# Kernel optimization log

Hardware: AMD Instinct MI355X
Metric: run time of the kernel (lower is better)

## Reference

```python
import jax, jax.numpy as jnp
import numpy as np

N_USER, N_VIDEO, N_PUB, N_TAG = 200000, 100000, 20000, 5000
EMB = 128
HALF = EMB // 2
LAYER_NUM = 3


def setup_inputs() -> dict:
    key = jax.random.key(0)
    ks = jax.random.split(key, 20)
    inp = {
        "user_emb": jax.random.normal(ks[0], (N_USER, EMB), jnp.float32),
        "video_emb": jax.random.normal(ks[1], (N_VIDEO, EMB), jnp.float32),
        "publisher_emb": jax.random.normal(ks[2], (N_PUB, EMB), jnp.float32),
        "tag_emb": jax.random.normal(ks[3], (N_TAG, EMB), jnp.float32),
    }
    # (name, E, n_src, n_dst)
    rels = [
        ("uv", 1500000, N_USER, N_VIDEO),
        ("vu", 1500000, N_VIDEO, N_USER),
        ("up", 800000, N_USER, N_PUB),
        ("pu", 800000, N_PUB, N_USER),
        ("vt", 800000, N_VIDEO, N_TAG),
        ("tv", 800000, N_TAG, N_VIDEO),
        ("pt", 400000, N_PUB, N_TAG),
        ("tp", 400000, N_TAG, N_PUB),
    ]
    for i, (name, E, ns, nd) in enumerate(rels):
        inp[name + "_src"] = jax.random.randint(ks[4 + 2 * i], (E,), 0, ns, jnp.int32)
        inp[name + "_dst"] = jax.random.randint(ks[5 + 2 * i], (E,), 0, nd, jnp.int32)
    return inp


def _seg_mean(feat, src, dst, num_dst):
    # copy_u + mean: gather half-dim src features, segment-mean onto dst.
    msg = feat[src]                                             # [E, HALF]
    s = jax.ops.segment_sum(msg, dst, num_segments=num_dst)     # [num_dst, HALF]
    deg = jax.ops.segment_sum(jnp.ones_like(dst, dtype=feat.dtype), dst,
                              num_segments=num_dst)
    return s / jnp.maximum(deg, 1.0)[:, None]  # zero-in-degree nodes -> 0 (DGL behavior)


def reference(user_emb, video_emb, publisher_emb, tag_emb,
              uv_src, uv_dst, vu_src, vu_dst,
              up_src, up_dst, pu_src, pu_dst,
              vt_src, vt_dst, tv_src, tv_dst,
              pt_src, pt_dst, tp_src, tp_dst):

    def layer(u, v, p, t):
        # user dst: [vu, pu]; video dst: [uv, tv]; publisher dst: [up, tp]; tag dst: [vt, pt]
        vu = _seg_mean(v[:, :HALF], vu_src, vu_dst, N_USER)
        pu = _seg_mean(p[:, :HALF], pu_src, pu_dst, N_USER)
        uv = _seg_mean(u[:, :HALF], uv_src, uv_dst, N_VIDEO)
        tv = _seg_mean(t[:, :HALF], tv_src, tv_dst, N_VIDEO)
        up = _seg_mean(u[:, HALF:], up_src, up_dst, N_PUB)
        tp = _seg_mean(t[:, HALF:], tp_src, tp_dst, N_PUB)
        vt = _seg_mean(v[:, HALF:], vt_src, vt_dst, N_TAG)
        pt = _seg_mean(p[:, HALF:], pt_src, pt_dst, N_TAG)
        return (jnp.concatenate([vu, pu], axis=1),
                jnp.concatenate([uv, tv], axis=1),
                jnp.concatenate([up, tp], axis=1),
                jnp.concatenate([vt, pt], axis=1))

    pu_, pv_, pp_, pt_ = user_emb, video_emb, publisher_emb, tag_emb
    u, v, p, t = user_emb, video_emb, publisher_emb, tag_emb
    for i in range(LAYER_NUM):
        u, v, p, t = layer(u, v, p, t)
        w = 1.0 / (i + 2)
        pu_ = pu_ + u * w
        pv_ = pv_ + v * w
        pp_ = pp_ + p * w
        pt_ = pt_ + t * w
    return (pu_, pv_, pp_, pt_)
```

## Files before the change

kernel.cpp:

```cpp
#include <hip/hip_runtime.h>
#include <stdint.h>

#define EMB 128
#define PCAP 12288
#define SCAP 13312

static constexpr int N_USER = 200000, N_VIDEO = 100000, N_PUB = 20000, N_TAG = 5000;
static constexpr int ROW_U = 0, ROW_V = 200000, ROW_P = 300000, ROW_T = 320000;
static constexpr int ROWS = 325000;
static constexpr int TOTAL_E = 7000000;
static constexpr int TOTAL_GROUPS = 650000;
static constexpr int TILE = 8192;
static constexpr int SORT_MAX = TOTAL_E + 7 * TOTAL_GROUPS;

using f32x4 = __attribute__((ext_vector_type(4))) float;
using u32x4 = __attribute__((ext_vector_type(4))) unsigned int;
using u32x2 = __attribute__((ext_vector_type(2))) unsigned int;

__device__ inline unsigned bf16_rne(float f) {
  unsigned u = __float_as_uint(f);
  return (u + 0x7fffu + ((u >> 16) & 1u)) >> 16;
}
__device__ inline unsigned pack_bf16x2(float lo, float hi) {
  return bf16_rne(lo) | (bf16_rne(hi) << 16);
}

__device__ inline unsigned fp8enc(float f) {
  unsigned b = __float_as_uint(f);
  unsigned s = (b >> 24) & 0x80u;
  unsigned ae = b & 0x7FFFFFFFu;
  unsigned r = ae + 0x7FFFFu + ((ae >> 20) & 1u);
  unsigned e = r >> 23;
  if (e < 121u) {
    float av = __uint_as_float(ae);
    unsigned m = (unsigned)__builtin_rintf(av * 512.0f);
    return s | m;
  }
  return s | ((e - 120u) << 3) | ((r >> 20) & 7u);
}
#if __has_builtin(__builtin_amdgcn_cvt_f32_fp8)
#define DEC4(w, x0, x1, x2, x3) \
  x0 += __builtin_amdgcn_cvt_f32_fp8((int)(w), 0); \
  x1 += __builtin_amdgcn_cvt_f32_fp8((int)(w), 1); \
  x2 += __builtin_amdgcn_cvt_f32_fp8((int)(w), 2); \
  x3 += __builtin_amdgcn_cvt_f32_fp8((int)(w), 3);
#else
__device__ inline float fp8dec(unsigned b) {
  unsigned s = (b & 0x80u) << 24;
  unsigned e = (b >> 3) & 0xFu;
  unsigned m = b & 7u;
  if (e == 0) { float f = (float)m * 0.001953125f; return s ? -f : f; }
  return __uint_as_float(s | ((e + 120u) << 23) | (m << 20));
}
#define DEC4(w, x0, x1, x2, x3) \
  x0 += fp8dec((w) & 0xffu); x1 += fp8dec(((w) >> 8) & 0xffu); \
  x2 += fp8dec(((w) >> 16) & 0xffu); x3 += fp8dec(((w) >> 24) & 0xffu);
#endif

struct SortDesc {
  int tcum[9];
  int bcum[9];
  int gcum[8];
  int E[8];
  int n_dst[8];
  int wshift[8];
  int zrow[8];
  const int* esrc[8];
  const int* edst[8];
};

struct AggrDesc {
  int cum[9];
  int src_base[8];
  int src_col[8];
  int dst_base[8];
  int dst_col[8];
  const float* demb[8];
};

__global__ __launch_bounds__(256) void part_kernel(SortDesc d, unsigned* __restrict__ pairs,
                                                   int* __restrict__ cursors) {
  __shared__ int cnt[256];
  __shared__ int lcur[256];
  int blk = blockIdx.x;
  int r = 0;
#pragma unroll
  for (int k = 1; k < 8; ++k) if (blk >= d.tcum[k]) r = k;
  int base = (blk - d.tcum[r]) * TILE;
  int n = min(TILE, d.E[r] - base);
  const int* __restrict__ esrc = d.esrc[r];
  const int* __restrict__ edst = d.edst[r];
  int tid = threadIdx.x;
  int B = d.bcum[r + 1] - d.bcum[r];
  int sh = d.wshift[r];
  int msk = (1 << sh) - 1;
  int bb = d.bcum[r];
  if (tid < B) cnt[tid] = 0;
  __syncthreads();
  for (int i = tid; i < n; i += 256)
    atomicAdd(&cnt[edst[base + i] >> sh], 1);
  __syncthreads();
  if (tid < B) {
    int c = cnt[tid];
    lcur[tid] = c ? atomicAdd(&cursors[bb + tid], c) : 0;
  }
  __syncthreads();
  for (int i = tid; i < n; i += 256) {
    int dv = edst[base + i];
    int sv = esrc[base + i];
    int b = dv >> sh;
    int pos = atomicAdd(&lcur[b], 1);
    if (pos < PCAP)
      pairs[(size_t)(bb + b) * PCAP + pos] = ((unsigned)(dv & msk) << 18) | (unsigned)sv;
  }
}

__global__ __launch_bounds__(256) void build_kernel(SortDesc d, const unsigned* __restrict__ pairs,
                                                    const int* __restrict__ cursors,
                                                    int* __restrict__ gcounter,
                                                    int* __restrict__ sorted,
                                                    int* __restrict__ Beg, int* __restrict__ Deg) {
  __shared__ int cnt[1024];
  __shared__ int poff[1025];
  __shared__ int stage[SCAP];
  __shared__ int wsums[4];
  __shared__ int sh_gbase;
  int bucket = blockIdx.x;
  int r = 0;
#pragma unroll
  for (int k = 1; k < 8; ++k) if (bucket >= d.bcum[k]) r = k;
  int bl = bucket - d.bcum[r];
  int sh = d.wshift[r];
  int first = bl << sh;
  int Wa = min(1 << sh, d.n_dst[r] - first);
  int zr = d.zrow[r];
  int tid = threadIdx.x;
  int n_b = min(cursors[bucket], PCAP);
  const unsigned* __restrict__ bp = pairs + (size_t)bucket * PCAP;

  for (int i = tid; i < 1024; i += 256) cnt[i] = 0;
  __syncthreads();
  for (int i = tid; i < n_b; i += 256)
    atomicAdd(&cnt[bp[i] >> 18], 1);
  __syncthreads();

  int t4 = tid * 4;
  int c0 = cnt[t4], c1 = cnt[t4 + 1], c2 = cnt[t4 + 2], c3 = cnt[t4 + 3];
  int p0 = (c0 + 7) & ~7, p1 = (c1 + 7) & ~7, p2 = (c2 + 7) & ~7, p3 = (c3 + 7) & ~7;
  int s = p0 + p1 + p2 + p3;
  int lane = tid & 63, wv = tid >> 6;
  int v = s;
#pragma unroll
  for (int dd = 1; dd < 64; dd <<= 1) {
    int t = __shfl_up(v, dd);
    if (lane >= dd) v += t;
  }
  if (lane == 63) wsums[wv] = v;
  __syncthreads();
  if (tid == 0) {
    int run = 0;
#pragma unroll
    for (int k = 0; k < 4; ++k) { int t = wsums[k]; wsums[k] = run; run += t; }
  }
  __syncthreads();
  int ex = wsums[wv] + (v - s);
  if (tid == 255) {
    int tot = ex + s;
    sh_gbase = atomicAdd(gcounter, tot);
    poff[1024] = min(tot, SCAP);
  }
  __syncthreads();
  int gbase = sh_gbase;
  int o0 = ex, o1 = ex + p0, o2 = o1 + p1, o3 = o2 + p2;
  cnt[t4] = o0; cnt[t4 + 1] = o1; cnt[t4 + 2] = o2; cnt[t4 + 3] = o3;
  poff[t4] = o0; poff[t4 + 1] = o1; poff[t4 + 2] = o2; poff[t4 + 3] = o3;
  int g0 = d.gcum[r] + first + t4;
  if (t4 + 0 < Wa) { Beg[g0 + 0] = gbase + o0; Deg[g0 + 0] = c0; }
  if (t4 + 1 < Wa) { Beg[g0 + 1] = gbase + o1; Deg[g0 + 1] = c1; }
  if (t4 + 2 < Wa) { Beg[g0 + 2] = gbase + o2; Deg[g0 + 2] = c2; }
  if (t4 + 3 < Wa) { Beg[g0 + 3] = gbase + o3; Deg[g0 + 3] = c3; }
  __syncthreads();

  for (int i = tid; i < n_b; i += 256) {
    unsigned pr = bp[i];
    int pos = atomicAdd(&cnt[pr >> 18], 1);
    if (pos < SCAP) stage[pos] = (int)(pr & 0x3FFFFu);
  }
  __syncthreads();
#pragma unroll
  for (int jj = 0; jj < 4; ++jj) {
    int j = t4 + jj;
    int end_ = min((j < 1023) ? poff[j + 1] : poff[1024], SCAP);
    for (int k = cnt[j]; k < end_; ++k) stage[k] = zr;
  }
  __syncthreads();

  int tot = poff[1024];
  for (int i = tid; i < tot; i += 256)
    sorted[gbase + i] = stage[i];
}

__global__ void convert_kernel(const float* __restrict__ u, const float* __restrict__ v,
                               const float* __restrict__ p, const float* __restrict__ t,
                               uint16_t* __restrict__ featA, uint16_t* __restrict__ featB,
                               unsigned char* __restrict__ f1f8) {
  int idx = blockIdx.x * blockDim.x + threadIdx.x;
  const int total8 = (ROWS + 1) * EMB / 8;
  if (idx >= total8) return;
  int flat = idx * 8;
  int row = flat >> 7;
  if (row == ROWS) {
    uint4 z = {0u, 0u, 0u, 0u};
    *(uint4*)(featA + flat) = z;
    *(uint4*)(featB + flat) = z;
    if (f1f8) { uint2 z2 = {0u, 0u}; *(uint2*)(f1f8 + flat) = z2; }
    return;
  }
  int col = flat & 127;
  const float* s;
  if (row < ROW_V)      s = u + (size_t)row * EMB + col;
  else if (row < ROW_P) s = v + (size_t)(row - ROW_V) * EMB + col;
  else if (row < ROW_T) s = p + (size_t)(row - ROW_P) * EMB + col;
  else                  s = t + (size_t)(row - ROW_T) * EMB + col;
  float4 f0 = *(const float4*)s;
  float4 f1 = *((const float4*)s + 1);
  uint4 o;
  o.x = pack_bf16x2(f0.x, f0.y);
  o.y = pack_bf16x2(f0.z, f0.w);
  o.z = pack_bf16x2(f1.x, f1.y);
  o.w = pack_bf16x2(f1.z, f1.w);
  *(uint4*)(featA + flat) = o;
}

#define ACC(q) \
  a0 += __uint_as_float((q).x << 16); a1 += __uint_as_float((q).x & 0xffff0000u); \
  a2 += __uint_as_float((q).y << 16); a3 += __uint_as_float((q).y & 0xffff0000u); \
  a4 += __uint_as_float((q).z << 16); a5 += __uint_as_float((q).z & 0xffff0000u); \
  a6 += __uint_as_float((q).w << 16); a7 += __uint_as_float((q).w & 0xffff0000u);

#define ACC8(qq) \
  DEC4((qq).x, a0, a1, a2, a3); DEC4((qq).y, a4, a5, a6, a7);

template<int M>
__global__ __launch_bounds__(256) void aggr_kernel(AggrDesc d,
    const uint16_t* __restrict__ gsrc_bf, const unsigned char* __restrict__ gsrc_f8,
    uint16_t* __restrict__ dst_bf, unsigned char* __restrict__ dst_f8,
    const uint16_t* __restrict__ f1_bf, const uint16_t* __restrict__ demb_bf,
    float* __restrict__ out,
    const int* __restrict__ sorted, const int* __restrict__ Beg,
    const int* __restrict__ Deg) {
  if ((M == 1 || M == 3) && blockIdx.x == 0 && threadIdx.x < 16) {
    uint2 z = {0u, 0u};
    *(uint2*)(dst_f8 + (size_t)ROWS * EMB + threadIdx.x * 8) = z;
  }
  int g = blockIdx.x * 32 + (threadIdx.x >> 3);
  if (g >= TOTAL_GROUPS) return;
  int lane = threadIdx.x & 7;
  int r = 0;
#pragma unroll
  for (int k = 1; k < 8; ++k) if (g >= d.cum[k]) r = k;
  int n = g - d.cum[r];
  int beg = Beg[g], dg = Deg[g];
  float recip = 1.0f / (float)(dg > 0 ? dg : 1);
  constexpr bool GB = (M == 0 || M == 3 || M == 4);
  const uint16_t* __restrict__ sb16 =
      GB ? gsrc_bf + (size_t)d.src_base[r] * EMB + d.src_col[r] + lane * 8 : nullptr;
  const unsigned char* __restrict__ sb8 =
      !GB ? gsrc_f8 + (size_t)d.src_base[r] * EMB + d.src_col[r] + lane * 8 : nullptr;
  float a0 = 0.f, a1 = 0.f, a2 = 0.f, a3 = 0.f, a4 = 0.f, a5 = 0.f, a6 = 0.f, a7 = 0.f;
  int nchunk = (dg + 7) >> 3;
  const int* ep = sorted + beg;
  int4 iA0 = {0,0,0,0}, iA1 = {0,0,0,0};
  if (nchunk > 0) { iA0 = *(const int4*)ep; iA1 = *(const int4*)(ep + 4); }
  for (int c = 0; c < nchunk; ++c) {
    int4 iB0 = {0,0,0,0}, iB1 = {0,0,0,0};
    if (c + 1 < nchunk) { iB0 = *(const int4*)(ep + 8); iB1 = *(const int4*)(ep + 12); }
    if (GB) {
      uint4 q0 = *(const uint4*)(sb16 + (size_t)iA0.x * EMB);
      uint4 q1 = *(const uint4*)(sb16 + (size_t)iA0.y * EMB);
      uint4 q2 = *(const uint4*)(sb16 + (size_t)iA0.z * EMB);
      uint4 q3 = *(const uint4*)(sb16 + (size_t)iA0.w * EMB);
      uint4 q4 = *(const uint4*)(sb16 + (size_t)iA1.x * EMB);
      uint4 q5 = *(const uint4*)(sb16 + (size_t)iA1.y * EMB);
      uint4 q6 = *(const uint4*)(sb16 + (size_t)iA1.z * EMB);
      uint4 q7 = *(const uint4*)(sb16 + (size_t)iA1.w * EMB);
      __builtin_amdgcn_sched_barrier(0);
      ACC(q0); ACC(q1); ACC(q2); ACC(q3);
      ACC(q4); ACC(q5); ACC(q6); ACC(q7);
    } else {
      uint2 q0 = *(const uint2*)(sb8 + (size_t)iA0.x * EMB);
      uint2 q1 = *(const uint2*)(sb8 + (size_t)iA0.y * EMB);
      uint2 q2 = *(const uint2*)(sb8 + (size_t)iA0.z * EMB);
      uint2 q3 = *(const uint2*)(sb8 + (size_t)iA0.w * EMB);
      uint2 q4 = *(const uint2*)(sb8 + (size_t)iA1.x * EMB);
      uint2 q5 = *(const uint2*)(sb8 + (size_t)iA1.y * EMB);
      uint2 q6 = *(const uint2*)(sb8 + (size_t)iA1.z * EMB);
      uint2 q7 = *(const uint2*)(sb8 + (size_t)iA1.w * EMB);
      __builtin_amdgcn_sched_barrier(0);
      ACC8(q0); ACC8(q1); ACC8(q2); ACC8(q3);
      ACC8(q4); ACC8(q5); ACC8(q6); ACC8(q7);
    }
    iA0 = iB0; iA1 = iB1; ep += 8;
  }
  a0 *= recip; a1 *= recip; a2 *= recip; a3 *= recip;
  a4 *= recip; a5 *= recip; a6 *= recip; a7 *= recip;

  int col = d.dst_col[r] + lane * 8;
  size_t dpos = (size_t)(d.dst_base[r] + n) * EMB + col;

  if (M == 0 || M == 4) {
    u32x4 ov;
    ov.x = pack_bf16x2(a0, a1);
    ov.y = pack_bf16x2(a2, a3);
    ov.z = pack_bf16x2(a4, a5);
    ov.w = pack_bf16x2(a6, a7);
    __builtin_nontemporal_store(ov, (u32x4*)(dst_bf + dpos));
    if (M == 4) {
      u32x2 o8;
      o8.x = fp8enc(a0) | (fp8enc(a1) << 8) | (fp8enc(a2) << 16) | (fp8enc(a3) << 24);
      o8.y = fp8enc(a4) | (fp8enc(a5) << 8) | (fp8enc(a6) << 16) | (fp8enc(a7) << 24);
      __builtin_nontemporal_store(o8, (u32x2*)(dst_f8 + dpos));
    }
    return;
  }
  if (M == 1 || M == 3) {
    u32x2 ov;
    ov.x = fp8enc(a0) | (fp8enc(a1) << 8) | (fp8enc(a2) << 16) | (fp8enc(a3) << 24);
    ov.y = fp8enc(a4) | (fp8enc(a5) << 8) | (fp8enc(a6) << 16) | (fp8enc(a7) << 24);
    __builtin_nontemporal_store(ov, (u32x2*)(dst_f8 + dpos));
    return;
  }

  u32x4 q1 = __builtin_nontemporal_load((const u32x4*)(f1_bf + dpos));
  u32x2 qf = __builtin_nontemporal_load((const u32x2*)(gsrc_f8 + dpos));
  float g0 = 0.f, g1 = 0.f, g2 = 0.f, g3 = 0.f, g4 = 0.f, g5 = 0.f, g6 = 0.f, g7 = 0.f;
  DEC4(qf.x, g0, g1, g2, g3);
  DEC4(qf.y, g4, g5, g6, g7);
  f32x4 v0, v1;
  if (demb_bf) {
    u32x4 qe = __builtin_nontemporal_load((const u32x4*)(demb_bf + dpos));
    v0.x = __uint_as_float(qe.x << 16); v0.y = __uint_as_float(qe.x & 0xffff0000u);
    v0.z = __uint_as_float(qe.y << 16); v0.w = __uint_as_float(qe.y & 0xffff0000u);
    v1.x = __uint_as_float(qe.z << 16); v1.y = __uint_as_float(qe.z & 0xffff0000u);
    v1.z = __uint_as_float(qe.w << 16); v1.w = __uint_as_float(qe.w & 0xffff0000u);
  } else {
    const f32x4* de = (const f32x4*)(d.demb[r] + (size_t)n * EMB + col);
    v0 = __builtin_nontemporal_load(de);
    v1 = __builtin_nontemporal_load(de + 1);
  }
  const float w1 = 0.5f, w2 = 1.0f / 3.0f, w3 = 0.25f;
  v0.x += w1 * __uint_as_float(q1.x << 16)         + w2 * g0 + w3 * a0;
  v0.y += w1 * __uint_as_float(q1.x & 0xffff0000u) + w2 * g1 + w3 * a1;
  v0.z += w1 * __uint_as_float(q1.y << 16)         + w2 * g2 + w3 * a2;
  v0.w += w1 * __uint_as_float(q1.y & 0xffff0000u) + w2 * g3 + w3 * a3;
  v1.x += w1 * __uint_as_float(q1.z << 16)         + w2 * g4 + w3 * a4;
  v1.y += w1 * __uint_as_float(q1.z & 0xffff0000u) + w2 * g5 + w3 * a5;
  v1.z += w1 * __uint_as_float(q1.w << 16)         + w2 * g6 + w3 * a6;
  v1.w += w1 * __uint_as_float(q1.w & 0xffff0000u) + w2 * g7 + w3 * a7;
  __builtin_nontemporal_store(v0, (f32x4*)(out + dpos));
  __builtin_nontemporal_store(v1, (f32x4*)(out + dpos) + 1);
}

extern "C" void kernel_launch(void* const* d_in, const int* in_sizes, int n_in,
                              void* d_out, int out_size, void* d_ws, size_t ws_size,
                              hipStream_t stream) {
  const float* emb_u = (const float*)d_in[0];
  const float* emb_v = (const float*)d_in[1];
  const float* emb_p = (const float*)d_in[2];
  const float* emb_t = (const float*)d_in[3];

  struct RelInfo { int si, di, E, n_dst, src_base, src_col, dst_base, dst_col, wshift; };
  const RelInfo rels[8] = {
    {12, 13,  800000, N_TAG,   ROW_V, 64, ROW_T,  0,  5},
    {16, 17,  400000, N_TAG,   ROW_P, 64, ROW_T, 64,  5},
    { 8,  9,  800000, N_PUB,   ROW_U, 64, ROW_P,  0,  7},
    {18, 19,  400000, N_PUB,   ROW_T, 64, ROW_P, 64,  7},
    { 4,  5, 1500000, N_VIDEO, ROW_U,  0, ROW_V,  0,  9},
    {14, 15,  800000, N_VIDEO, ROW_T,  0, ROW_V, 64,  9},
    { 6,  7, 1500000, N_USER,  ROW_V,  0, ROW_U,  0, 10},
    {10, 11,  800000, N_USER,  ROW_P,  0, ROW_U, 64, 10},
  };
  const float* dembs[8] = {emb_t, emb_t, emb_p, emb_p, emb_v, emb_v, emb_u, emb_u};

  char* ws = (char*)d_ws;
  size_t cursor = 0;
  auto take = [&](size_t bytes) -> char* {
    char* p = ws + cursor;
    cursor = (cursor + bytes + 255) & ~(size_t)255;
    return p;
  };
  uint16_t* featA = (uint16_t*)take((size_t)(ROWS + 1) * EMB * 2);
  uint16_t* featB = (uint16_t*)take((size_t)(ROWS + 1) * EMB * 2);
  int* sorted = (int*)take((size_t)SORT_MAX * 4);
  int* Beg    = (int*)take((size_t)TOTAL_GROUPS * 4);
  int* Deg    = (int*)take((size_t)TOTAL_GROUPS * 4);
  unsigned* pairs = (unsigned*)d_ws;

  SortDesc sd;
  AggrDesc ad;
  int tacc = 0, bacc = 0, gacc = 0;
  for (int r = 0; r < 8; ++r) {
    int n_dst = rels[r].n_dst;
    sd.tcum[r] = tacc; tacc += (rels[r].E + TILE - 1) / TILE;
    sd.bcum[r] = bacc; bacc += (n_dst + (1 << rels[r].wshift) - 1) >> rels[r].wshift;
    sd.gcum[r] = gacc;
    sd.E[r] = rels[r].E;
    sd.n_dst[r] = n_dst;
    sd.wshift[r] = rels[r].wshift;
    sd.zrow[r] = ROWS - rels[r].src_base;
    sd.esrc[r] = (const int*)d_in[rels[r].si];
    sd.edst[r] = (const int*)d_in[rels[r].di];

    ad.cum[r] = gacc;
    ad.src_base[r] = rels[r].src_base;
    ad.src_col[r] = rels[r].src_col;
    ad.dst_base[r] = rels[r].dst_base;
    ad.dst_col[r] = rels[r].dst_col;
    ad.demb[r] = dembs[r];
    gacc += n_dst;
  }
  sd.tcum[8] = tacc;
  sd.bcum[8] = bacc;
  ad.cum[8] = gacc;

  int* cursors  = (int*)take((size_t)bacc * 4 + 4);
  int* gcounter = cursors + bacc;

  const size_t f8bytes = (size_t)(ROWS + 1) * EMB;
  size_t base_need = cursor;
  unsigned char* f1fp8 = nullptr;
  unsigned char* f2fp8 = (unsigned char*)featA;
  bool use_fp8_l1 = false;
  const uint16_t* demb_bf = nullptr;
  if (ws_size >= base_need + f8bytes + 256) {
    f1fp8 = (unsigned char*)take(f8bytes);
    use_fp8_l1 = true;
    if (ws_size >= cursor + f8bytes + 256) {
      f2fp8 = (unsigned char*)take(f8bytes);
      demb_bf = featA;
    }
  }

  hipMemsetAsync(cursors, 0, (size_t)(bacc + 1) * 4, stream);
  part_kernel<<<tacc, 256, 0, stream>>>(sd, pairs, cursors);
  build_kernel<<<bacc, 256, 0, stream>>>(sd, pairs, cursors, gcounter, sorted, Beg, Deg);

  convert_kernel<<<((ROWS + 1) * EMB / 8 + 255) / 256, 256, 0, stream>>>(
      emb_u, emb_v, emb_p, emb_t, featA, featB, f1fp8);

  float* out = (float*)d_out;
  const int aggr_blocks = (TOTAL_GROUPS + 31) / 32;
  if (use_fp8_l1) {
    aggr_kernel<4><<<aggr_blocks, 256, 0, stream>>>(ad, featA, nullptr, featB, f1fp8,
                                                    nullptr, nullptr, nullptr, sorted, Beg, Deg);
    aggr_kernel<1><<<aggr_blocks, 256, 0, stream>>>(ad, nullptr, f1fp8, nullptr, f2fp8,
                                                    nullptr, nullptr, nullptr, sorted, Beg, Deg);
  } else {
    aggr_kernel<0><<<aggr_blocks, 256, 0, stream>>>(ad, featA, nullptr, featB, nullptr,
                                                    nullptr, nullptr, nullptr, sorted, Beg, Deg);
    aggr_kernel<3><<<aggr_blocks, 256, 0, stream>>>(ad, featB, nullptr, nullptr, f2fp8,
                                                    nullptr, nullptr, nullptr, sorted, Beg, Deg);
  }
  aggr_kernel<2><<<aggr_blocks, 256, 0, stream>>>(ad, nullptr, f2fp8, nullptr, nullptr,
                                                  featB, demb_bf, out, sorted, Beg, Deg);
}
```

Baseline: 599.6 us.

## Aggregate both relations per destination node in one thread group with 4-aligned padding

Result: slower. 612.2 us (+2.1%).

```diff
diff --git a/kernel.cpp b/kernel.cpp
--- a/kernel.cpp
+++ b/kernel.cpp
@@ -3,19 +3,21 @@
 
 #define EMB 128
 #define PCAP 12288
-#define SCAP 13312
+#define SCAP 14336
 
 static constexpr int N_USER = 200000, N_VIDEO = 100000, N_PUB = 20000, N_TAG = 5000;
 static constexpr int ROW_U = 0, ROW_V = 200000, ROW_P = 300000, ROW_T = 320000;
 static constexpr int ROWS = 325000;
+static constexpr int NODES = 325000;
 static constexpr int TOTAL_E = 7000000;
 static constexpr int TOTAL_GROUPS = 650000;
 static constexpr int TILE = 8192;
-static constexpr int SORT_MAX = TOTAL_E + 7 * TOTAL_GROUPS;
+static constexpr int SORT_MAX = TOTAL_E + 3 * TOTAL_GROUPS + 64;
 
 using f32x4 = __attribute__((ext_vector_type(4))) float;
 using u32x4 = __attribute__((ext_vector_type(4))) unsigned int;
 using u32x2 = __attribute__((ext_vector_type(2))) unsigned int;
+using i32x4 = __attribute__((ext_vector_type(4))) int;
 
 __device__ inline unsigned bf16_rne(float f) {
   unsigned u = __float_as_uint(f);
@@ -60,7 +62,7 @@
 struct SortDesc {
   int tcum[9];
   int bcum[9];
-  int gcum[8];
+  int nbase[8];
   int E[8];
   int n_dst[8];
   int wshift[8];
@@ -70,12 +72,9 @@
 };
 
 struct AggrDesc {
-  int cum[9];
-  int src_base[8];
-  int src_col[8];
-  int dst_base[8];
-  int dst_col[8];
-  const float* demb[8];
+  int ncum1, ncum2, ncum3;
+  int sb0[4], sb1[4], dstb[4];
+  const float* demb[4];
 };
 
 __global__ __launch_bounds__(256) void part_kernel(SortDesc d, unsigned* __restrict__ pairs,
@@ -119,7 +118,7 @@
                                                     const int* __restrict__ cursors,
                                                     int* __restrict__ gcounter,
                                                     int* __restrict__ sorted,
-                                                    int* __restrict__ Beg, int* __restrict__ Deg) {
+                                                    int* __restrict__ BegDeg) {
   __shared__ int cnt[1024];
   __shared__ int poff[1025];
   __shared__ int stage[SCAP];
@@ -134,6 +133,8 @@
   int first = bl << sh;
   int Wa = min(1 << sh, d.n_dst[r] - first);
   int zr = d.zrow[r];
+  int half = r & 1;
+  int nb0 = d.nbase[r] + first;
   int tid = threadIdx.x;
   int n_b = min(cursors[bucket], PCAP);
   const unsigned* __restrict__ bp = pairs + (size_t)bucket * PCAP;
@@ -146,7 +147,7 @@
 
   int t4 = tid * 4;
   int c0 = cnt[t4], c1 = cnt[t4 + 1], c2 = cnt[t4 + 2], c3 = cnt[t4 + 3];
-  int p0 = (c0 + 7) & ~7, p1 = (c1 + 7) & ~7, p2 = (c2 + 7) & ~7, p3 = (c3 + 7) & ~7;
+  int p0 = (c0 + 3) & ~3, p1 = (c1 + 3) & ~3, p2 = (c2 + 3) & ~3, p3 = (c3 + 3) & ~3;
   int s = p0 + p1 + p2 + p3;
   int lane = tid & 63, wv = tid >> 6;
   int v = s;
@@ -174,11 +175,11 @@
   int o0 = ex, o1 = ex + p0, o2 = o1 + p1, o3 = o2 + p2;
   cnt[t4] = o0; cnt[t4 + 1] = o1; cnt[t4 + 2] = o2; cnt[t4 + 3] = o3;
   poff[t4] = o0; poff[t4 + 1] = o1; poff[t4 + 2] = o2; poff[t4 + 3] = o3;
-  int g0 = d.gcum[r] + first + t4;
-  if (t4 + 0 < Wa) { Beg[g0 + 0] = gbase + o0; Deg[g0 + 0] = c0; }
-  if (t4 + 1 < Wa) { Beg[g0 + 1] = gbase + o1; Deg[g0 + 1] = c1; }
-  if (t4 + 2 < Wa) { Beg[g0 + 2] = gbase + o2; Deg[g0 + 2] = c2; }
-  if (t4 + 3 < Wa) { Beg[g0 + 3] = gbase + o3; Deg[g0 + 3] = c3; }
+  int2* bd = (int2*)BegDeg;
+  if (t4 + 0 < Wa) bd[(size_t)(nb0 + t4 + 0) * 2 + half] = make_int2(gbase + o0, c0);
+  if (t4 + 1 < Wa) bd[(size_t)(nb0 + t4 + 1) * 2 + half] = make_int2(gbase + o1, c1);
+  if (t4 + 2 < Wa) bd[(size_t)(nb0 + t4 + 2) * 2 + half] = make_int2(gbase + o2, c2);
+  if (t4 + 3 < Wa) bd[(size_t)(nb0 + t4 + 3) * 2 + half] = make_int2(gbase + o3, c3);
   __syncthreads();
 
   for (int i = tid; i < n_b; i += 256) {
@@ -232,14 +233,77 @@
   *(uint4*)(featA + flat) = o;
 }
 
-#define ACC(q) \
+#define ACCQ(q) \
   a0 += __uint_as_float((q).x << 16); a1 += __uint_as_float((q).x & 0xffff0000u); \
   a2 += __uint_as_float((q).y << 16); a3 += __uint_as_float((q).y & 0xffff0000u); \
   a4 += __uint_as_float((q).z << 16); a5 += __uint_as_float((q).z & 0xffff0000u); \
   a6 += __uint_as_float((q).w << 16); a7 += __uint_as_float((q).w & 0xffff0000u);
 
-#define ACC8(qq) \
+#define ACC8Q(qq) \
   DEC4((qq).x, a0, a1, a2, a3); DEC4((qq).y, a4, a5, a6, a7);
+
+template<bool GB>
+__device__ __forceinline__ void run_list(const uint16_t* __restrict__ sb16,
+                                         const unsigned char* __restrict__ sb8,
+                                         const int* __restrict__ ep, int dg,
+                                         i32x4 i0, i32x4 i1,
+                                         float& a0, float& a1, float& a2, float& a3,
+                                         float& a4, float& a5, float& a6, float& a7) {
+  int P = (dg + 3) & ~3;
+  int n8 = P >> 3, has4 = P & 4;
+  for (int c = 0; c < n8; ++c) {
+    i32x4 j0 = {0, 0, 0, 0}, j1 = {0, 0, 0, 0};
+    if (c + 1 < n8) {
+      j0 = __builtin_nontemporal_load((const i32x4*)(ep + 8));
+      j1 = __builtin_nontemporal_load((const i32x4*)(ep + 8) + 1);
+    } else if (has4) {
+      j0 = __builtin_nontemporal_load((const i32x4*)(ep + 8));
+    }
+    if (GB) {
+      uint4 q0 = *(const uint4*)(sb16 + (size_t)i0[0] * EMB);
+      uint4 q1 = *(const uint4*)(sb16 + (size_t)i0[1] * EMB);
+      uint4 q2 = *(const uint4*)(sb16 + (size_t)i0[2] * EMB);
+      uint4 q3 = *(const uint4*)(sb16 + (size_t)i0[3] * EMB);
+      uint4 q4 = *(const uint4*)(sb16 + (size_t)i1[0] * EMB);
+      uint4 q5 = *(const uint4*)(sb16 + (size_t)i1[1] * EMB);
+      uint4 q6 = *(const uint4*)(sb16 + (size_t)i1[2] * EMB);
+      uint4 q7 = *(const uint4*)(sb16 + (size_t)i1[3] * EMB);
+      __builtin_amdgcn_sched_barrier(0);
+      ACCQ(q0); ACCQ(q1); ACCQ(q2); ACCQ(q3);
+      ACCQ(q4); ACCQ(q5); ACCQ(q6); ACCQ(q7);
+    } else {
+      uint2 q0 = *(const uint2*)(sb8 + (size_t)i0[0] * EMB);
+      uint2 q1 = *(const uint2*)(sb8 + (size_t)i0[1] * EMB);
+      uint2 q2 = *(const uint2*)(sb8 + (size_t)i0[2] * EMB);
+      uint2 q3 = *(const uint2*)(sb8 + (size_t)i0[3] * EMB);
+      uint2 q4 = *(const uint2*)(sb8 + (size_t)i1[0] * EMB);
+      uint2 q5 = *(const uint2*)(sb8 + (size_t)i1[1] * EMB);
+      uint2 q6 = *(const uint2*)(sb8 + (size_t)i1[2] * EMB);
+      uint2 q7 = *(const uint2*)(sb8 + (size_t)i1[3] * EMB);
+      __builtin_amdgcn_sched_barrier(0);
+      ACC8Q(q0); ACC8Q(q1); ACC8Q(q2); ACC8Q(q3);
+      ACC8Q(q4); ACC8Q(q5); ACC8Q(q6); ACC8Q(q7);
+    }
+    i0 = j0; i1 = j1; ep += 8;
+  }
+  if (has4) {
+    if (GB) {
+      uint4 q0 = *(const uint4*)(sb16 + (size_t)i0[0] * EMB);
+      uint4 q1 = *(const uint4*)(sb16 + (size_t)i0[1] * EMB);
+      uint4 q2 = *(const uint4*)(sb16 + (size_t)i0[2] * EMB);
+      uint4 q3 = *(const uint4*)(sb16 + (size_t)i0[3] * EMB);
+      __builtin_amdgcn_sched_barrier(0);
+      ACCQ(q0); ACCQ(q1); ACCQ(q2); ACCQ(q3);
+    } else {
+      uint2 q0 = *(const uint2*)(sb8 + (size_t)i0[0] * EMB);
+      uint2 q1 = *(const uint2*)(sb8 + (size_t)i0[1] * EMB);
+      uint2 q2 = *(const uint2*)(sb8 + (size_t)i0[2] * EMB);
+      uint2 q3 = *(const uint2*)(sb8 + (size_t)i0[3] * EMB);
+      __builtin_amdgcn_sched_barrier(0);
+      ACC8Q(q0); ACC8Q(q1); ACC8Q(q2); ACC8Q(q3);
+    }
+  }
+}
 
 template<int M>
 __global__ __launch_bounds__(256) void aggr_kernel(AggrDesc d,
@@ -247,118 +311,133 @@
     uint16_t* __restrict__ dst_bf, unsigned char* __restrict__ dst_f8,
     const uint16_t* __restrict__ f1_bf, const uint16_t* __restrict__ demb_bf,
     float* __restrict__ out,
-    const int* __restrict__ sorted, const int* __restrict__ Beg,
-    const int* __restrict__ Deg) {
+    const int* __restrict__ sorted, const int* __restrict__ BegDeg) {
   if ((M == 1 || M == 3) && blockIdx.x == 0 && threadIdx.x < 16) {
     uint2 z = {0u, 0u};
     *(uint2*)(dst_f8 + (size_t)ROWS * EMB + threadIdx.x * 8) = z;
   }
-  int g = blockIdx.x * 32 + (threadIdx.x >> 3);
-  if (g >= TOTAL_GROUPS) return;
+  int node = blockIdx.x * 32 + (threadIdx.x >> 3);
+  if (node >= NODES) return;
   int lane = threadIdx.x & 7;
-  int r = 0;
-#pragma unroll
-  for (int k = 1; k < 8; ++k) if (g >= d.cum[k]) r = k;
-  int n = g - d.cum[r];
-  int beg = Beg[g], dg = Deg[g];
-  float recip = 1.0f / (float)(dg > 0 ? dg : 1);
+  int t = (node >= d.ncum1) + (node >= d.ncum2) + (node >= d.ncum3);
+  int n = node - ((t == 0) ? 0 : (t == 1) ? d.ncum1 : (t == 2) ? d.ncum2 : d.ncum3);
+  const int4 bd = *(const int4*)(BegDeg + (size_t)node * 4);
+  int scol = (t < 2) ? 64 : 0;
   constexpr bool GB = (M == 0 || M == 3 || M == 4);
-  const uint16_t* __restrict__ sb16 =
-      GB ? gsrc_bf + (size_t)d.src_base[r] * EMB + d.src_col[r] + lane * 8 : nullptr;
-  const unsigned char* __restrict__ sb8 =
-      !GB ? gsrc_f8 + (size_t)d.src_base[r] * EMB + d.src_col[r] + lane * 8 : nullptr;
+  const uint16_t* __restrict__ s16_0 =
+      GB ? gsrc_bf + (size_t)d.sb0[t] * EMB + scol + lane * 8 : nullptr;
+  const uint16_t* __restrict__ s16_1 =
+      GB ? gsrc_bf + (size_t)d.sb1[t] * EMB + scol + lane * 8 : nullptr;
+  const unsigned char* __restrict__ s8_0 =
+      !GB ? gsrc_f8 + (size_t)d.sb0[t] * EMB + scol + lane * 8 : nullptr;
+  const unsigned char* __restrict__ s8_1 =
+      !GB ? gsrc_f8 + (size_t)d.sb1[t] * EMB + scol + lane * 8 : nullptr;
+
+  const int* epA = sorted + bd.x;
+  const int* epB = sorted + bd.z;
+  i32x4 ia0 = {0,0,0,0}, ia1 = {0,0,0,0}, ib0 = {0,0,0,0}, ib1 = {0,0,0,0};
+  if (bd.y > 0) {
+    ia0 = __builtin_nontemporal_load((const i32x4*)epA);
+    ia1 = __builtin_nontemporal_load((const i32x4*)epA + 1);
+  }
+  if (bd.w > 0) {
+    ib0 = __builtin_nontemporal_load((const i32x4*)epB);
+    ib1 = __builtin_nontemporal_load((const i32x4*)epB + 1);
+  }
+
   float a0 = 0.f, a1 = 0.f, a2 = 0.f, a3 = 0.f, a4 = 0.f, a5 = 0.f, a6 = 0.f, a7 = 0.f;
-  int nchunk = (dg + 7) >> 3;
-  const int* ep = sorted + beg;
-  int4 iA0 = {0,0,0,0}, iA1 = {0,0,0,0};
-  if (nchunk > 0) { iA0 = *(const int4*)ep; iA1 = *(const int4*)(ep + 4); }
-  for (int c = 0; c < nchunk; ++c) {
-    int4 iB0 = {0,0,0,0}, iB1 = {0,0,0,0};
-    if (c + 1 < nchunk) { iB0 = *(const int4*)(ep + 8); iB1 = *(const int4*)(ep + 12); }
-    if (GB) {
-      uint4 q0 = *(const uint4*)(sb16 + (size_t)iA0.x * EMB);
-      uint4 q1 = *(const uint4*)(sb16 + (size_t)iA0.y * EMB);
-      uint4 q2 = *(const uint4*)(sb16 + (size_t)iA0.z * EMB);
-      uint4 q3 = *(const uint4*)(sb16 + (size_t)iA0.w * EMB);
-      uint4 q4 = *(const uint4*)(sb16 + (size_t)iA1.x * EMB);
-      uint4 q5 = *(const uint4*)(sb16 + (size_t)iA1.y * EMB);
-      uint4 q6 = *(const uint4*)(sb16 + (size_t)iA1.z * EMB);
-      uint4 q7 = *(const uint4*)(sb16 + (size_t)iA1.w * EMB);
-      __builtin_amdgcn_sched_barrier(0);
-      ACC(q0); ACC(q1); ACC(q2); ACC(q3);
-      ACC(q4); ACC(q5); ACC(q6); ACC(q7);
-    } else {
-      uint2 q0 = *(const uint2*)(sb8 + (size_t)iA0.x * EMB);
-      uint2 q1 = *(const uint2*)(sb8 + (size_t)iA0.y * EMB);
-      uint2 q2 = *(const uint2*)(sb8 + (size_t)iA0.z * EMB);
-      uint2 q3 = *(const uint2*)(sb8 + (size_t)iA0.w * EMB);
-      uint2 q4 = *(const uint2*)(sb8 + (size_t)iA1.x * EMB);
-      uint2 q5 = *(const uint2*)(sb8 + (size_t)iA1.y * EMB);
-      uint2 q6 = *(const uint2*)(sb8 + (size_t)iA1.z * EMB);
-      uint2 q7 = *(const uint2*)(sb8 + (size_t)iA1.w * EMB);
-      __builtin_amdgcn_sched_barrier(0);
-      ACC8(q0); ACC8(q1); ACC8(q2); ACC8(q3);
-      ACC8(q4); ACC8(q5); ACC8(q6); ACC8(q7);
-    }
-    iA0 = iB0; iA1 = iB1; ep += 8;
-  }
-  a0 *= recip; a1 *= recip; a2 *= recip; a3 *= recip;
-  a4 *= recip; a5 *= recip; a6 *= recip; a7 *= recip;
-
-  int col = d.dst_col[r] + lane * 8;
-  size_t dpos = (size_t)(d.dst_base[r] + n) * EMB + col;
+  run_list<GB>(s16_0, s8_0, epA, bd.y, ia0, ia1, a0, a1, a2, a3, a4, a5, a6, a7);
+  float b0 = 0.f, b1 = 0.f, b2 = 0.f, b3 = 0.f, b4 = 0.f, b5 = 0.f, b6 = 0.f, b7 = 0.f;
+  run_list<GB>(s16_1, s8_1, epB, bd.w, ib0, ib1, b0, b1, b2, b3, b4, b5, b6, b7);
+
+  float rA = 1.0f / (float)(bd.y > 0 ? bd.y : 1);
+  float rB = 1.0f / (float)(bd.w > 0 ? bd.w : 1);
+  a0 *= rA; a1 *= rA; a2 *= rA; a3 *= rA; a4 *= rA; a5 *= rA; a6 *= rA; a7 *= rA;
+  b0 *= rB; b1 *= rB; b2 *= rB; b3 *= rB; b4 *= rB; b5 *= rB; b6 *= rB; b7 *= rB;
+
+  size_t drow = (size_t)(d.dstb[t] + n) * EMB;
+  size_t dp0 = drow + lane * 8;
+  size_t dp1 = dp0 + 64;
 
   if (M == 0 || M == 4) {
-    u32x4 ov;
-    ov.x = pack_bf16x2(a0, a1);
-    ov.y = pack_bf16x2(a2, a3);
-    ov.z = pack_bf16x2(a4, a5);
-    ov.w = pack_bf16x2(a6, a7);
-    __builtin_nontemporal_store(ov, (u32x4*)(dst_bf + dpos));
+    u32x4 oa, ob;
+    oa.x = pack_bf16x2(a0, a1); oa.y = pack_bf16x2(a2, a3);
+    oa.z = pack_bf16x2(a4, a5); oa.w = pack_bf16x2(a6, a7);
+    ob.x = pack_bf16x2(b0, b1); ob.y = pack_bf16x2(b2, b3);
+    ob.z = pack_bf16x2(b4, b5); ob.w = pack_bf16x2(b6, b7);
+    __builtin_nontemporal_store(oa, (u32x4*)(dst_bf + dp0));
+    __builtin_nontemporal_store(ob, (u32x4*)(dst_bf + dp1));
     if (M == 4) {
-      u32x2 o8;
-      o8.x = fp8enc(a0) | (fp8enc(a1) << 8) | (fp8enc(a2) << 16) | (fp8enc(a3) << 24);
-      o8.y = fp8enc(a4) | (fp8enc(a5) << 8) | (fp8enc(a6) << 16) | (fp8enc(a7) << 24);
-      __builtin_nontemporal_store(o8, (u32x2*)(dst_f8 + dpos));
+      u32x2 fa, fb;
+      fa.x = fp8enc(a0) | (fp8enc(a1) << 8) | (fp8enc(a2) << 16) | (fp8enc(a3) << 24);
+      fa.y = fp8enc(a4) | (fp8enc(a5) << 8) | (fp8enc(a6) << 16) | (fp8enc(a7) << 24);
+      fb.x = fp8enc(b0) | (fp8enc(b1) << 8) | (fp8enc(b2) << 16) | (fp8enc(b3) << 24);
+      fb.y = fp8enc(b4) | (fp8enc(b5) << 8) | (fp8enc(b6) << 16) | (fp8enc(b7) << 24);
+      __builtin_nontemporal_store(fa, (u32x2*)(dst_f8 + dp0));
+      __builtin_nontemporal_store(fb, (u32x2*)(dst_f8 + dp1));
     }
     return;
   }
   if (M == 1 || M == 3) {
-    u32x2 ov;
-    ov.x = fp8enc(a0) | (fp8enc(a1) << 8) | (fp8enc(a2) << 16) | (fp8enc(a3) << 24);
-    ov.y = fp8enc(a4) | (fp8enc(a5) << 8) | (fp8enc(a6) << 16) | (fp8enc(a7) << 24);
-    __builtin_nontemporal_store(ov, (u32x2*)(dst_f8 + dpos));
+    u32x2 fa, fb;
+    fa.x = fp8enc(a0) | (fp8enc(a1) << 8) | (fp8enc(a2) << 16) | (fp8enc(a3) << 24);
+    fa.y = fp8enc(a4) | (fp8enc(a5) << 8) | (fp8enc(a6) << 16) | (fp8enc(a7) << 24);
+    fb.x = fp8enc(b0) | (fp8enc(b1) << 8) | (fp8enc(b2) << 16) | (fp8enc(b3) << 24);
+    fb.y = fp8enc(b4) | (fp8enc(b5) << 8) | (fp8enc(b6) << 16) | (fp8enc(b7) << 24);
+    __builtin_nontemporal_store(fa, (u32x2*)(dst_f8 + dp0));
+    __builtin_nontemporal_store(fb, (u32x2*)(dst_f8 + dp1));
     return;
   }
 
-  u32x4 q1 = __builtin_nontemporal_load((const u32x4*)(f1_bf + dpos));
-  u32x2 qf = __builtin_nontemporal_load((const u32x2*)(gsrc_f8 + dpos));
-  float g0 = 0.f, g1 = 0.f, g2 = 0.f, g3 = 0.f, g4 = 0.f, g5 = 0.f, g6 = 0.f, g7 = 0.f;
-  DEC4(qf.x, g0, g1, g2, g3);
-  DEC4(qf.y, g4, g5, g6, g7);
-  f32x4 v0, v1;
+  const float w1 = 0.5f, w2 = 1.0f / 3.0f, w3 = 0.25f;
+  u32x4 q1a = __builtin_nontemporal_load((const u32x4*)(f1_bf + dp0));
+  u32x4 q1b = __builtin_nontemporal_load((const u32x4*)(f1_bf + dp1));
+  u32x2 qfa = __builtin_nontemporal_load((const u32x2*)(gsrc_f8 + dp0));
+  u32x2 qfb = __builtin_nontemporal_load((const u32x2*)(gsrc_f8 + dp1));
+  float g0=0.f,g1=0.f,g2=0.f,g3=0.f,g4=0.f,g5=0.f,g6=0.f,g7=0.f;
+  float h0=0.f,h1=0.f,h2=0.f,h3=0.f,h4=0.f,h5=0.f,h6=0.f,h7=0.f;
+  DEC4(qfa.x, g0, g1, g2, g3); DEC4(qfa.y, g4, g5, g6, g7);
+  DEC4(qfb.x, h0, h1, h2, h3); DEC4(qfb.y, h4, h5, h6, h7);
+  f32x4 v0, v1, v2, v3;
   if (demb_bf) {
-    u32x4 qe = __builtin_nontemporal_load((const u32x4*)(demb_bf + dpos));
-    v0.x = __uint_as_float(qe.x << 16); v0.y = __uint_as_float(qe.x & 0xffff0000u);
-    v0.z = __uint_as_float(qe.y << 16); v0.w = __uint_as_float(qe.y & 0xffff0000u);
-    v1.x = __uint_as_float(qe.z << 16); v1.y = __uint_as_float(qe.z & 0xffff0000u);
-    v1.z = __uint_as_float(qe.w << 16); v1.w = __uint_as_float(qe.w & 0xffff0000u);
+    u32x4 qea = __builtin_nontemporal_load((const u32x4*)(demb_bf + dp0));
+    u32x4 qeb = __builtin_nontemporal_load((const u32x4*)(demb_bf + dp1));
+    v0.x = __uint_as_float(qea.x << 16); v0.y = __uint_as_float(qea.x & 0xffff0000u);
+    v0.z = __uint_as_float(qea.y << 16); v0.w = __uint_as_float(qea.y & 0xffff0000u);
+    v1.x = __uint_as_float(qea.z << 16); v1.y = __uint_as_float(qea.z & 0xffff0000u);
+    v1.z = __uint_as_float(qea.w << 16); v1.w = __uint_as_float(qea.w & 0xffff0000u);
+    v2.x = __uint_as_float(qeb.x << 16); v2.y = __uint_as_float(qeb.x & 0xffff0000u);
+    v2.z = __uint_as_float(qeb.y << 16); v2.w = __uint_as_float(qeb.y & 0xffff0000u);
+    v3.x = __uint_as_float(qeb.z << 16); v3.y = __uint_as_float(qeb.z & 0xffff0000u);
+    v3.z = __uint_as_float(qeb.w << 16); v3.w = __uint_as_float(qeb.w & 0xffff0000u);
   } else {
-    const f32x4* de = (const f32x4*)(d.demb[r] + (size_t)n * EMB + col);
+    const f32x4* de = (const f32x4*)(d.demb[t] + (size_t)n * EMB + lane * 8);
     v0 = __builtin_nontemporal_load(de);
     v1 = __builtin_nontemporal_load(de + 1);
-  }
-  const float w1 = 0.5f, w2 = 1.0f / 3.0f, w3 = 0.25f;
-  v0.x += w1 * __uint_as_float(q1.x << 16)         + w2 * g0 + w3 * a0;
-  v0.y += w1 * __uint_as_float(q1.x & 0xffff0000u) + w2 * g1 + w3 * a1;
-  v0.z += w1 * __uint_as_float(q1.y << 16)         + w2 * g2 + w3 * a2;
-  v0.w += w1 * __uint_as_float(q1.y & 0xffff0000u) + w2 * g3 + w3 * a3;
-  v1.x += w1 * __uint_as_float(q1.z << 16)         + w2 * g4 + w3 * a4;
-  v1.y += w1 * __uint_as_float(q1.z & 0xffff0000u) + w2 * g5 + w3 * a5;
-  v1.z += w1 * __uint_as_float(q1.w << 16)         + w2 * g6 + w3 * a6;
-  v1.w += w1 * __uint_as_float(q1.w & 0xffff0000u) + w2 * g7 + w3 * a7;
-  __builtin_nontemporal_store(v0, (f32x4*)(out + dpos));
-  __builtin_nontemporal_store(v1, (f32x4*)(out + dpos) + 1);
+    const f32x4* de1 = (const f32x4*)(d.demb[t] + (size_t)n * EMB + 64 + lane * 8);
+    v2 = __builtin_nontemporal_load(de1);
+    v3 = __builtin_nontemporal_load(de1 + 1);
+  }
+  v0.x += w1 * __uint_as_float(q1a.x << 16)         + w2 * g0 + w3 * a0;
+  v0.y += w1 * __uint_as_float(q1a.x & 0xffff0000u) + w2 * g1 + w3 * a1;
+  v0.z += w1 * __uint_as_float(q1a.y << 16)         + w2 * g2 + w3 * a2;
+  v0.w += w1 * __uint_as_float(q1a.y & 0xffff0000u) + w2 * g3 + w3 * a3;
+  v1.x += w1 * __uint_as_float(q1a.z << 16)         + w2 * g4 + w3 * a4;
+  v1.y += w1 * __uint_as_float(q1a.z & 0xffff0000u) + w2 * g5 + w3 * a5;
+  v1.z += w1 * __uint_as_float(q1a.w << 16)         + w2 * g6 + w3 * a6;
+  v1.w += w1 * __uint_as_float(q1a.w & 0xffff0000u) + w2 * g7 + w3 * a7;
+  v2.x += w1 * __uint_as_float(q1b.x << 16)         + w2 * h0 + w3 * b0;
+  v2.y += w1 * __uint_as_float(q1b.x & 0xffff0000u) + w2 * h1 + w3 * b1;
+  v2.z += w1 * __uint_as_float(q1b.y << 16)         + w2 * h2 + w3 * b2;
+  v2.w += w1 * __uint_as_float(q1b.y & 0xffff0000u) + w2 * h3 + w3 * b3;
+  v3.x += w1 * __uint_as_float(q1b.z << 16)         + w2 * h4 + w3 * b4;
+  v3.y += w1 * __uint_as_float(q1b.z & 0xffff0000u) + w2 * h5 + w3 * b5;
+  v3.z += w1 * __uint_as_float(q1b.w << 16)         + w2 * h6 + w3 * b6;
+  v3.w += w1 * __uint_as_float(q1b.w & 0xffff0000u) + w2 * h7 + w3 * b7;
+  __builtin_nontemporal_store(v0, (f32x4*)(out + dp0));
+  __builtin_nontemporal_store(v1, (f32x4*)(out + dp0) + 1);
+  __builtin_nontemporal_store(v2, (f32x4*)(out + dp1));
+  __builtin_nontemporal_store(v3, (f32x4*)(out + dp1) + 1);
 }
 
 extern "C" void kernel_launch(void* const* d_in, const int* in_sizes, int n_in,
@@ -369,18 +448,18 @@
   const float* emb_p = (const float*)d_in[2];
   const float* emb_t = (const float*)d_in[3];
 
-  struct RelInfo { int si, di, E, n_dst, src_base, src_col, dst_base, dst_col, wshift; };
+  struct RelInfo { int si, di, E, n_dst, src_base, dst_base, wshift; };
   const RelInfo rels[8] = {
-    {12, 13,  800000, N_TAG,   ROW_V, 64, ROW_T,  0,  5},
-    {16, 17,  400000, N_TAG,   ROW_P, 64, ROW_T, 64,  5},
-    { 8,  9,  800000, N_PUB,   ROW_U, 64, ROW_P,  0,  7},
-    {18, 19,  400000, N_PUB,   ROW_T, 64, ROW_P, 64,  7},
-    { 4,  5, 1500000, N_VIDEO, ROW_U,  0, ROW_V,  0,  9},
-    {14, 15,  800000, N_VIDEO, ROW_T,  0, ROW_V, 64,  9},
-    { 6,  7, 1500000, N_USER,  ROW_V,  0, ROW_U,  0, 10},
-    {10, 11,  800000, N_USER,  ROW_P,  0, ROW_U, 64, 10},
+    {12, 13,  800000, N_TAG,   ROW_V, ROW_T,  5},
+    {16, 17,  400000, N_TAG,   ROW_P, ROW_T,  5},
+    { 8,  9,  800000, N_PUB,   ROW_U, ROW_P,  7},
+    {18, 19,  400000, N_PUB,   ROW_T, ROW_P,  7},
+    { 4,  5, 1500000, N_VIDEO, ROW_U, ROW_V,  9},
+    {14, 15,  800000, N_VIDEO, ROW_T, ROW_V,  9},
+    { 6,  7, 1500000, N_USER,  ROW_V, ROW_U, 10},
+    {10, 11,  800000, N_USER,  ROW_P, ROW_U, 10},
   };
-  const float* dembs[8] = {emb_t, emb_t, emb_p, emb_p, emb_v, emb_v, emb_u, emb_u};
+  const int ncum[5] = {0, N_TAG, N_TAG + N_PUB, N_TAG + N_PUB + N_VIDEO, NODES};
 
   char* ws = (char*)d_ws;
   size_t cursor = 0;
@@ -391,37 +470,34 @@
   };
   uint16_t* featA = (uint16_t*)take((size_t)(ROWS + 1) * EMB * 2);
   uint16_t* featB = (uint16_t*)take((size_t)(ROWS + 1) * EMB * 2);
-  int* sorted = (int*)take((size_t)SORT_MAX * 4);
-  int* Beg    = (int*)take((size_t)TOTAL_GROUPS * 4);
-  int* Deg    = (int*)take((size_t)TOTAL_GROUPS * 4);
+  int* sorted  = (int*)take((size_t)SORT_MAX * 4);
+  int* BegDeg  = (int*)take((size_t)NODES * 16);
   unsigned* pairs = (unsigned*)d_ws;
 
   SortDesc sd;
   AggrDesc ad;
-  int tacc = 0, bacc = 0, gacc = 0;
+  int tacc = 0, bacc = 0;
   for (int r = 0; r < 8; ++r) {
-    int n_dst = rels[r].n_dst;
     sd.tcum[r] = tacc; tacc += (rels[r].E + TILE - 1) / TILE;
-    sd.bcum[r] = bacc; bacc += (n_dst + (1 << rels[r].wshift) - 1) >> rels[r].wshift;
-    sd.gcum[r] = gacc;
+    sd.bcum[r] = bacc; bacc += (rels[r].n_dst + (1 << rels[r].wshift) - 1) >> rels[r].wshift;
+    sd.nbase[r] = ncum[r >> 1];
     sd.E[r] = rels[r].E;
-    sd.n_dst[r] = n_dst;
+    sd.n_dst[r] = rels[r].n_dst;
     sd.wshift[r] = rels[r].wshift;
     sd.zrow[r] = ROWS - rels[r].src_base;
     sd.esrc[r] = (const int*)d_in[rels[r].si];
     sd.edst[r] = (const int*)d_in[rels[r].di];
-
-    ad.cum[r] = gacc;
-    ad.src_base[r] = rels[r].src_base;
-    ad.src_col[r] = rels[r].src_col;
-    ad.dst_base[r] = rels[r].dst_base;
-    ad.dst_col[r] = rels[r].dst_col;
-    ad.demb[r] = dembs[r];
-    gacc += n_dst;
   }
   sd.tcum[8] = tacc;
   sd.bcum[8] = bacc;
-  ad.cum[8] = gacc;
+
+  ad.ncum1 = ncum[1]; ad.ncum2 = ncum[2]; ad.ncum3 = ncum[3];
+  for (int t = 0; t < 4; ++t) {
+    ad.sb0[t]  = rels[2 * t].src_base;
+    ad.sb1[t]  = rels[2 * t + 1].src_base;
+    ad.dstb[t] = rels[2 * t].dst_base;
+  }
+  ad.demb[0] = emb_t; ad.demb[1] = emb_p; ad.demb[2] = emb_v; ad.demb[3] = emb_u;
 
   int* cursors  = (int*)take((size_t)bacc * 4 + 4);
   int* gcounter = cursors + bacc;
@@ -443,24 +519,24 @@
 
   hipMemsetAsync(cursors, 0, (size_t)(bacc + 1) * 4, stream);
   part_kernel<<<tacc, 256, 0, stream>>>(sd, pairs, cursors);
-  build_kernel<<<bacc, 256, 0, stream>>>(sd, pairs, cursors, gcounter, sorted, Beg, Deg);
+  build_kernel<<<bacc, 256, 0, stream>>>(sd, pairs, cursors, gcounter, sorted, BegDeg);
 
   convert_kernel<<<((ROWS + 1) * EMB / 8 + 255) / 256, 256, 0, stream>>>(
       emb_u, emb_v, emb_p, emb_t, featA, featB, f1fp8);
 
   float* out = (float*)d_out;
-  const int aggr_blocks = (TOTAL_GROUPS + 31) / 32;
+  const int aggr_blocks = (NODES + 31) / 32;
   if (use_fp8_l1) {
     aggr_kernel<4><<<aggr_blocks, 256, 0, stream>>>(ad, featA, nullptr, featB, f1fp8,
-                                                    nullptr, nullptr, nullptr, sorted, Beg, Deg);
+                                                    nullptr, nullptr, nullptr, sorted, BegDeg);
     aggr_kernel<1><<<aggr_blocks, 256, 0, stream>>>(ad, nullptr, f1fp8, nullptr, f2fp8,
-                                                    nullptr, nullptr, nullptr, sorted, Beg, Deg);
+                                                    nullptr, nullptr, nullptr, sorted, BegDeg);
   } else {
     aggr_kernel<0><<<aggr_blocks, 256, 0, stream>>>(ad, featA, nullptr, featB, nullptr,
-                                                    nullptr, nullptr, nullptr, sorted, Beg, Deg);
+                                                    nullptr, nullptr, nullptr, sorted, BegDeg);
     aggr_kernel<3><<<aggr_blocks, 256, 0, stream>>>(ad, featB, nullptr, nullptr, f2fp8,
-                                                    nullptr, nullptr, nullptr, sorted, Beg, Deg);
+                                                    nullptr, nullptr, nullptr, sorted, BegDeg);
   }
   aggr_kernel<2><<<aggr_blocks, 256, 0, stream>>>(ad, nullptr, f2fp8, nullptr, nullptr,
-                                                  featB, demb_bf, out, sorted, Beg, Deg);
-}
+                                                  featB, demb_bf, out, sorted, BegDeg);
+}
```
